# Performance work log

Hardware: AMD Instinct MI355X
Metric: run time of the kernel (lower is better)

## Reference

```python
import jax, jax.numpy as jnp
import numpy as np

D_MODEL = 1024
N_HEADS = 16
D_HEAD = 64
BATCH = 4
SEQ = 2048
NEG = -1000000000.0


def setup_inputs() -> dict:
    key = jax.random.key(0)
    k1, k2, k3, k4, k5 = jax.random.split(key, 5)
    x = jax.random.normal(k1, (BATCH, SEQ, D_MODEL), dtype=jnp.float32)
    std = 0.02
    wq = jax.random.normal(k2, (N_HEADS, D_HEAD, D_MODEL), dtype=jnp.float32) * std
    wk = jax.random.normal(k3, (N_HEADS, D_HEAD, D_MODEL), dtype=jnp.float32) * std
    wv = jax.random.normal(k4, (N_HEADS, D_HEAD, D_MODEL), dtype=jnp.float32) * std
    wo = jax.random.normal(k5, (D_MODEL, N_HEADS * D_HEAD), dtype=jnp.float32) * std
    return {"x": x, "wq": wq, "wk": wk, "wv": wv, "wo": wo}


def reference(x, wq, wk, wv, wo):
    # x: [b, s, d_model]; wq/wk/wv: [h, d_head, d_model]; wo: [d_model, h*d_head]
    b, s, _ = x.shape
    scale = jnp.sqrt(jnp.asarray(D_HEAD, x.dtype))
    q = jnp.einsum('bsd,hed->bhse', x, wq)
    k = jnp.einsum('bsd,hed->bhse', x, wk)
    v = jnp.einsum('bsd,hed->bhse', x, wv)
    scores = jnp.einsum('bhse,bhte->bhst', q, k) / scale
    causal_mask = jnp.triu(jnp.ones((s, s), dtype=bool), k=1)
    scores = jnp.where(causal_mask, jnp.asarray(NEG, scores.dtype), scores)
    weights = jax.nn.softmax(scores, axis=-1)
    heads = jnp.einsum('bhst,bhte->bhse', weights, v)  # [b, h, s, d_head]
    concat = heads.transpose(0, 2, 1, 3).reshape(b, s, N_HEADS * D_HEAD)
    return concat @ wo.T
```

## Files before the change

### kernel.cpp

```cpp
#include <hip/hip_runtime.h>


#define DEV __device__ __forceinline__

typedef __attribute__((ext_vector_type(8))) __bf16 bf16x8;
typedef __attribute__((ext_vector_type(4))) float f32x4;
typedef unsigned short u16;

struct alignas(8) U16x4 { u16 x, y, z, w; };

DEV u16 f2bf(float f) {
  unsigned int u = __builtin_bit_cast(unsigned int, f);
  u = u + 0x7FFFu + ((u >> 16) & 1u);
  return (u16)(u >> 16);
}

DEV unsigned cvt_pk_bf16(float a, float b) {
  unsigned r;
  asm("v_cvt_pk_bf16_f32 %0, %1, %2" : "=v"(r) : "v"(a), "v"(b));
  return r;
}

DEV void gload_lds16(const void* g, void* l) {
  __builtin_amdgcn_global_load_lds(
      (const __attribute__((address_space(1))) unsigned int*)g,
      (__attribute__((address_space(3))) unsigned int*)l, 16, 0, 0);
}

__global__ void cast_kernel(const float* __restrict__ in, u16* __restrict__ out, int n4) {
  int i = blockIdx.x * blockDim.x + threadIdx.x;
  if (i >= n4) return;
  const float4 v = reinterpret_cast<const float4*>(in)[i];
  U16x4 o{f2bf(v.x), f2bf(v.y), f2bf(v.z), f2bf(v.w)};
  reinterpret_cast<U16x4*>(out)[i] = o;
}

__global__ void cast_w_kernel(const float* __restrict__ wq, const float* __restrict__ wk,
                              const float* __restrict__ wv, const float* __restrict__ wo,
                              u16* __restrict__ wqkvb, u16* __restrict__ wob) {
  const int y = blockIdx.y;
  const int i = blockIdx.x * blockDim.x + threadIdx.x;
  const float* src = (y == 0) ? wq : (y == 1) ? wk : (y == 2) ? wv : wo;
  u16* dst = (y < 3) ? (wqkvb + (size_t)y * 1048576) : wob;
  const float4 v = reinterpret_cast<const float4*>(src)[i];
  U16x4 o{f2bf(v.x), f2bf(v.y), f2bf(v.z), f2bf(v.w)};
  reinterpret_cast<U16x4*>(dst)[i] = o;
}

template <int MODE>
__global__ __launch_bounds__(256) void gemm_bt(
    const u16* __restrict__ A, const u16* __restrict__ B,
    void* __restrict__ C0, u16* __restrict__ vtp, int N) {
  constexpr int K = 1024;
  const int bm = blockIdx.y, bn = blockIdx.x;
  const int tid = threadIdx.x;
  const int w = tid >> 6, lane = tid & 63, lo = lane & 15, hi = lane >> 4;
  const int wm = w >> 1, wn = w & 1;

  __shared__ char lds[65536];
  char* sA = lds;
  char* sB = lds + 32768;

  const u16* Ag = A + (size_t)(bm * 128) * K;
  const u16* Bg = B + (size_t)(bn * 128) * K;

  f32x4 acc[4][4] = {};

  auto stage = [&](int buf, int k0) {
#pragma unroll
    for (int it = 0; it < 4; ++it) {
      const int L = (it * 4 + w) * 64 + lane;
      const int r = L >> 3, p = L & 7, c = p ^ (r & 7);
      gload_lds16(Ag + (size_t)r * K + k0 + c * 8, sA + buf * 16384 + (it * 4 + w) * 1024);
      gload_lds16(Bg + (size_t)r * K + k0 + c * 8, sB + buf * 16384 + (it * 4 + w) * 1024);
    }
  };

  stage(0, 0);
  __syncthreads();
  int cur = 0;
  for (int t = 0; t < 16; ++t) {
    if (t + 1 < 16) stage(cur ^ 1, (t + 1) * 64);
#pragma unroll
    for (int kc = 0; kc < 2; ++kc) {
      bf16x8 af[4], bfr[4];
#pragma unroll
      for (int m = 0; m < 4; ++m) {
        const int r = wm * 64 + m * 16 + lo;
        const int p = (kc * 4 + hi) ^ (r & 7);
        af[m] = *reinterpret_cast<const bf16x8*>(sA + cur * 16384 + r * 128 + p * 16);
      }
#pragma unroll
      for (int n = 0; n < 4; ++n) {
        const int r = wn * 64 + n * 16 + lo;
        const int p = (kc * 4 + hi) ^ (r & 7);
        bfr[n] = *reinterpret_cast<const bf16x8*>(sB + cur * 16384 + r * 128 + p * 16);
      }
#pragma unroll
      for (int m = 0; m < 4; ++m)
#pragma unroll
        for (int n = 0; n < 4; ++n)
          acc[m][n] = __builtin_amdgcn_mfma_f32_16x16x32_bf16(af[m], bfr[n], acc[m][n], 0, 0, 0);
    }
    __syncthreads();
    cur ^= 1;
  }

  const int colW = bn * 128 + wn * 64;
  const int rowW = bm * 128 + wm * 64;
  if (MODE == 0) {
    float* C = (float*)C0;
#pragma unroll
    for (int m = 0; m < 4; ++m)
#pragma unroll
      for (int n = 0; n < 4; ++n) {
        const int col = colW + n * 16 + lo;
        const int rb = rowW + m * 16 + hi * 4;
#pragma unroll
        for (int rg = 0; rg < 4; ++rg)
          C[(size_t)(rb + rg) * N + col] = acc[m][n][rg];
      }
  } else {
    u16* qkvp = (u16*)C0;
    if (bn * 128 < 2048) {
      const float qs = (bn < 8) ? 0.18033688011112042f : 1.0f;
#pragma unroll
      for (int m = 0; m < 4; ++m)
#pragma unroll
        for (int n = 0; n < 4; ++n) {
          const int col = colW + n * 16 + lo;
          const int rb = rowW + m * 16 + hi * 4;
#pragma unroll
          for (int rg = 0; rg < 4; ++rg)
            qkvp[(size_t)(rb + rg) * 2048 + col] = f2bf(acc[m][n][rg] * qs);
        }
    } else {
#pragma unroll
      for (int m = 0; m < 4; ++m)
#pragma unroll
        for (int n = 0; n < 4; ++n) {
          const int col = colW + n * 16 + lo;
          const int idx = col - 2048;
          const int hh = idx >> 6, e = idx & 63;
          const int rb = rowW + m * 16 + hi * 4;
          const int bb = rb >> 11, s = rb & 2047;
          U16x4 v4{f2bf(acc[m][n][0]), f2bf(acc[m][n][1]),
                   f2bf(acc[m][n][2]), f2bf(acc[m][n][3])};
          *reinterpret_cast<U16x4*>(vtp + ((size_t)((bb * 16 + hh) * 64 + e)) * 2048 + s) = v4;
        }
    }
  }
}

__global__ __launch_bounds__(256, 4) void attn_kernel(
    const u16* __restrict__ qkv, const u16* __restrict__ vt, u16* __restrict__ heads) {
  const int bx = blockIdx.x;
  const int bh = blockIdx.y;
  const int b = bh >> 4, h = bh & 15;
  const int tid = threadIdx.x;
  const int w = tid >> 6, lane = tid & 63, lo = lane & 15, hi = lane >> 4;

  __shared__ char lds[40960];
  char* sQP = lds;
  char* sK  = lds + 8192;
  char* sV  = lds + 24576;

  const u16* Kg = qkv + (size_t)(b * 2048) * 2048 + 1024 + h * 64;
  const u16* Vg = vt + (size_t)bh * 64 * 2048;

  auto stageKV = [&](int buf, int kv0) {
#pragma unroll
    for (int it = 0; it < 2; ++it) {
      const int L = (it * 4 + w) * 64 + lane;
      const int r = L >> 3, p = L & 7, c = p ^ (r & 7);
      gload_lds16(Kg + (size_t)(kv0 + r) * 2048 + c * 8, sK + buf * 8192 + (it * 4 + w) * 1024);
      gload_lds16(Vg + (size_t)r * 2048 + kv0 + c * 8, sV + buf * 8192 + (it * 4 + w) * 1024);
    }
  };

  char* sP = sQP + w * 2048;

  for (int rep = 0; rep < 2; ++rep) {
    const int qt = rep ? (31 - bx) : bx;
    const u16* Qg = qkv + (size_t)(b * 2048 + qt * 64) * 2048 + h * 64;

#pragma unroll
    for (int it = 0; it < 2; ++it) {
      const int L = (it * 4 + w) * 64 + lane;
      const int r = L >> 3, p = L & 7, c = p ^ (r & 7);
      gload_lds16(Qg + (size_t)r * 2048 + c * 8, sQP + (it * 4 + w) * 1024);
    }
    stageKV(0, 0);
    __syncthreads();

    bf16x8 qf[2];
#pragma unroll
    for (int kc = 0; kc < 2; ++kc) {
      const int r = w * 16 + lo;
      const int p = (kc * 4 + hi) ^ (r & 7);
      qf[kc] = *reinterpret_cast<const bf16x8*>(sQP + r * 128 + p * 16);
    }
    __syncthreads();

    float mreg = -1e30f, lrow = 0.f;
    f32x4 oacc[4] = {};

    const int nt = qt + 1;
    int cur = 0;
    for (int t = 0; t < nt; ++t) {
      if (t + 1 < nt) stageKV(cur ^ 1, (t + 1) * 64);

      f32x4 sa[4] = {};
#pragma unroll
      for (int kc = 0; kc < 2; ++kc) {
#pragma unroll
        for (int n = 0; n < 4; ++n) {
          const int r = n * 16 + lo;
          const int p = (kc * 4 + hi) ^ (r & 7);
          const bf16x8 kf = *reinterpret_cast<const bf16x8*>(sK + cur * 8192 + r * 128 + p * 16);
          sa[n] = __builtin_amdgcn_mfma_f32_16x16x32_bf16(kf, qf[kc], sa[n], 0, 0, 0);
        }
      }

      if (t == nt - 1) {
        const int q = w * 16 + lo;
#pragma unroll
        for (int n = 0; n < 4; ++n)
#pragma unroll
          for (int rg = 0; rg < 4; ++rg)
            if (n * 16 + hi * 4 + rg > q) sa[n][rg] = -1e9f;
      }

      float pm = sa[0][0];
#pragma unroll
      for (int n = 0; n < 4; ++n)
#pragma unroll
        for (int rg = 0; rg < 4; ++rg) pm = fmaxf(pm, sa[n][rg]);
      pm = fmaxf(pm, __shfl_xor(pm, 16));
      pm = fmaxf(pm, __shfl_xor(pm, 32));
      if (!__all(pm <= mreg + 8.0f)) {
        const float mn = fmaxf(mreg, pm);
        const float alpha = exp2f(mreg - mn);
        mreg = mn;
        lrow *= alpha;
#pragma unroll
        for (int ne = 0; ne < 4; ++ne)
#pragma unroll
          for (int rg = 0; rg < 4; ++rg) oacc[ne][rg] *= alpha;
      }
      float rs = 0.f;
#pragma unroll
      for (int n = 0; n < 4; ++n)
#pragma unroll
        for (int rg = 0; rg < 4; ++rg) {
          const float pv = exp2f(sa[n][rg] - mreg);
          sa[n][rg] = pv;
          rs += pv;
        }
      lrow += rs;

#pragma unroll
      for (int n = 0; n < 4; ++n) {
        const unsigned w0 = cvt_pk_bf16(sa[n][0], sa[n][1]);
        const unsigned w1 = cvt_pk_bf16(sa[n][2], sa[n][3]);
        const int Hp = 2 * (n & 1) + (hi >> 1);
        *reinterpret_cast<uint2*>(sP + (n >> 1) * 1024 + Hp * 256 +
                                  ((lo ^ Hp) << 4) + ((hi & 1) << 3)) = uint2{w0, w1};
      }
      asm volatile("s_waitcnt lgkmcnt(0)" ::: "memory");
      bf16x8 pf[2];
#pragma unroll
      for (int kc = 0; kc < 2; ++kc)
        pf[kc] = *reinterpret_cast<const bf16x8*>(sP + kc * 1024 + hi * 256 + ((lo ^ hi) << 4));

#pragma unroll
      for (int kc = 0; kc < 2; ++kc) {
#pragma unroll
        for (int ne = 0; ne < 4; ++ne) {
          const int r = ne * 16 + lo;
          const int p = (kc * 4 + hi) ^ (r & 7);
          const bf16x8 vf = *reinterpret_cast<const bf16x8*>(sV + cur * 8192 + r * 128 + p * 16);
          oacc[ne] = __builtin_amdgcn_mfma_f32_16x16x32_bf16(vf, pf[kc], oacc[ne], 0, 0, 0);
        }
      }
      __syncthreads();
      cur ^= 1;
    }

    float lsum = lrow;
    lsum += __shfl_xor(lsum, 16);
    lsum += __shfl_xor(lsum, 32);
    const float inv = 1.0f / lsum;
    const int q = qt * 64 + w * 16 + lo;
    u16* dst = heads + (size_t)(b * 2048 + q) * 1024 + h * 64;
#pragma unroll
    for (int ne = 0; ne < 4; ++ne) {
      const unsigned r0 = cvt_pk_bf16(oacc[ne][0] * inv, oacc[ne][1] * inv);
      const unsigned r1 = cvt_pk_bf16(oacc[ne][2] * inv, oacc[ne][3] * inv);
      *reinterpret_cast<uint2*>(dst + ne * 16 + hi * 4) = uint2{r0, r1};
    }
  }
}

extern "C" void kernel_launch(void* const* d_in, const int* in_sizes, int n_in,
                              void* d_out, int out_size, void* d_ws, size_t ws_size,
                              hipStream_t stream) {
  const float* x  = (const float*)d_in[0];
  const float* wq = (const float*)d_in[1];
  const float* wk = (const float*)d_in[2];
  const float* wv = (const float*)d_in[3];
  const float* wo = (const float*)d_in[4];

  char* ws = (char*)d_ws;
  u16* xb    = (u16*)(ws);
  u16* wqkvb = (u16*)(ws + 16777216);
  u16* wob   = (u16*)(ws + 23068672);
  u16* qkv   = (u16*)(ws + 25165824);
  u16* vtp   = (u16*)(ws + 58720256);
  u16* heads = (u16*)(ws + 75497472);

  cast_kernel<<<8192, 256, 0, stream>>>(x, xb, 2097152);
  cast_w_kernel<<<dim3(1024, 4), 256, 0, stream>>>(wq, wk, wv, wo, wqkvb, wob);

  gemm_bt<1><<<dim3(24, 64), 256, 0, stream>>>(xb, wqkvb, qkv, vtp, 3072);
  attn_kernel<<<dim3(16, 64), 256, 0, stream>>>(qkv, vtp, heads);
  gemm_bt<0><<<dim3(8, 64), 256, 0, stream>>>(heads, wob, d_out, nullptr, 1024);
}
```

Baseline: 193.6 us.

## Double attention query tile per block to 128 rows for K/V reuse

Each attention workgroup now processes 128 query rows (32 per wave, two 16-row groups) instead of 64, so every staged K/V tile feeds twice as many MFMAs and global K/V traffic per query is halved. The grid shrinks to 8x64 blocks with paired query tiles for causal load balance, LDS grows to 48KB, and the occupancy hint in launch bounds is dropped. s_setprio is added around the MFMA sections to favor matrix issue. The costs are higher register pressure, fewer blocks (512) that may underfill the GPU, and more masked work on the diagonal tiles.

```diff
diff --git a/kernel.cpp b/kernel.cpp
--- a/kernel.cpp
+++ b/kernel.cpp
@@ -152,7 +152,7 @@
   }
 }
 
-__global__ __launch_bounds__(256, 4) void attn_kernel(
+__global__ __launch_bounds__(256) void attn_kernel(
     const u16* __restrict__ qkv, const u16* __restrict__ vt, u16* __restrict__ heads) {
   const int bx = blockIdx.x;
   const int bh = blockIdx.y;
@@ -160,10 +160,10 @@
   const int tid = threadIdx.x;
   const int w = tid >> 6, lane = tid & 63, lo = lane & 15, hi = lane >> 4;
 
-  __shared__ char lds[40960];
+  __shared__ char lds[49152];
   char* sQP = lds;
-  char* sK  = lds + 8192;
-  char* sV  = lds + 24576;
+  char* sK  = lds + 16384;
+  char* sV  = lds + 32768;
 
   const u16* Kg = qkv + (size_t)(b * 2048) * 2048 + 1024 + h * 64;
   const u16* Vg = vt + (size_t)bh * 64 * 2048;
@@ -178,14 +178,14 @@
     }
   };
 
-  char* sP = sQP + w * 2048;
+  char* sP = sQP + w * 4096;
 
   for (int rep = 0; rep < 2; ++rep) {
-    const int qt = rep ? (31 - bx) : bx;
-    const u16* Qg = qkv + (size_t)(b * 2048 + qt * 64) * 2048 + h * 64;
-
-#pragma unroll
-    for (int it = 0; it < 2; ++it) {
+    const int qt = rep ? (15 - bx) : bx;
+    const u16* Qg = qkv + (size_t)(b * 2048 + qt * 128) * 2048 + h * 64;
+
+#pragma unroll
+    for (int it = 0; it < 4; ++it) {
       const int L = (it * 4 + w) * 64 + lane;
       const int r = L >> 3, p = L & 7, c = p ^ (r & 7);
       gload_lds16(Qg + (size_t)r * 2048 + c * 8, sQP + (it * 4 + w) * 1024);
@@ -193,24 +193,27 @@
     stageKV(0, 0);
     __syncthreads();
 
-    bf16x8 qf[2];
-#pragma unroll
-    for (int kc = 0; kc < 2; ++kc) {
-      const int r = w * 16 + lo;
-      const int p = (kc * 4 + hi) ^ (r & 7);
-      qf[kc] = *reinterpret_cast<const bf16x8*>(sQP + r * 128 + p * 16);
-    }
+    bf16x8 qf[2][2];
+#pragma unroll
+    for (int qg = 0; qg < 2; ++qg)
+#pragma unroll
+      for (int kc = 0; kc < 2; ++kc) {
+        const int r = w * 32 + qg * 16 + lo;
+        const int p = (kc * 4 + hi) ^ (r & 7);
+        qf[qg][kc] = *reinterpret_cast<const bf16x8*>(sQP + r * 128 + p * 16);
+      }
     __syncthreads();
 
-    float mreg = -1e30f, lrow = 0.f;
-    f32x4 oacc[4] = {};
-
-    const int nt = qt + 1;
+    float mreg[2] = {-1e30f, -1e30f}, lrow[2] = {0.f, 0.f};
+    f32x4 oacc[2][4] = {};
+
+    const int nt = 2 * (qt + 1);
     int cur = 0;
     for (int t = 0; t < nt; ++t) {
       if (t + 1 < nt) stageKV(cur ^ 1, (t + 1) * 64);
 
-      f32x4 sa[4] = {};
+      f32x4 sa[2][4] = {};
+      __builtin_amdgcn_s_setprio(1);
 #pragma unroll
       for (int kc = 0; kc < 2; ++kc) {
 #pragma unroll
@@ -218,61 +221,73 @@
           const int r = n * 16 + lo;
           const int p = (kc * 4 + hi) ^ (r & 7);
           const bf16x8 kf = *reinterpret_cast<const bf16x8*>(sK + cur * 8192 + r * 128 + p * 16);
-          sa[n] = __builtin_amdgcn_mfma_f32_16x16x32_bf16(kf, qf[kc], sa[n], 0, 0, 0);
-        }
-      }
-
-      if (t == nt - 1) {
-        const int q = w * 16 + lo;
+          sa[0][n] = __builtin_amdgcn_mfma_f32_16x16x32_bf16(kf, qf[0][kc], sa[0][n], 0, 0, 0);
+          sa[1][n] = __builtin_amdgcn_mfma_f32_16x16x32_bf16(kf, qf[1][kc], sa[1][n], 0, 0, 0);
+        }
+      }
+      __builtin_amdgcn_s_setprio(0);
+
+      if (t >= nt - 2) {
+#pragma unroll
+        for (int qg = 0; qg < 2; ++qg) {
+          const int q = qt * 128 + w * 32 + qg * 16 + lo;
+#pragma unroll
+          for (int n = 0; n < 4; ++n)
+#pragma unroll
+            for (int rg = 0; rg < 4; ++rg)
+              if (t * 64 + n * 16 + hi * 4 + rg > q) sa[qg][n][rg] = -1e9f;
+        }
+      }
+
+#pragma unroll
+      for (int qg = 0; qg < 2; ++qg) {
+        float pm = sa[qg][0][0];
 #pragma unroll
         for (int n = 0; n < 4; ++n)
 #pragma unroll
-          for (int rg = 0; rg < 4; ++rg)
-            if (n * 16 + hi * 4 + rg > q) sa[n][rg] = -1e9f;
-      }
-
-      float pm = sa[0][0];
-#pragma unroll
-      for (int n = 0; n < 4; ++n)
-#pragma unroll
-        for (int rg = 0; rg < 4; ++rg) pm = fmaxf(pm, sa[n][rg]);
-      pm = fmaxf(pm, __shfl_xor(pm, 16));
-      pm = fmaxf(pm, __shfl_xor(pm, 32));
-      if (!__all(pm <= mreg + 8.0f)) {
-        const float mn = fmaxf(mreg, pm);
-        const float alpha = exp2f(mreg - mn);
-        mreg = mn;
-        lrow *= alpha;
-#pragma unroll
-        for (int ne = 0; ne < 4; ++ne)
-#pragma unroll
-          for (int rg = 0; rg < 4; ++rg) oacc[ne][rg] *= alpha;
-      }
-      float rs = 0.f;
-#pragma unroll
-      for (int n = 0; n < 4; ++n)
-#pragma unroll
-        for (int rg = 0; rg < 4; ++rg) {
-          const float pv = exp2f(sa[n][rg] - mreg);
-          sa[n][rg] = pv;
-          rs += pv;
-        }
-      lrow += rs;
-
-#pragma unroll
-      for (int n = 0; n < 4; ++n) {
-        const unsigned w0 = cvt_pk_bf16(sa[n][0], sa[n][1]);
-        const unsigned w1 = cvt_pk_bf16(sa[n][2], sa[n][3]);
-        const int Hp = 2 * (n & 1) + (hi >> 1);
-        *reinterpret_cast<uint2*>(sP + (n >> 1) * 1024 + Hp * 256 +
-                                  ((lo ^ Hp) << 4) + ((hi & 1) << 3)) = uint2{w0, w1};
+          for (int rg = 0; rg < 4; ++rg) pm = fmaxf(pm, sa[qg][n][rg]);
+        pm = fmaxf(pm, __shfl_xor(pm, 16));
+        pm = fmaxf(pm, __shfl_xor(pm, 32));
+        if (!__all(pm <= mreg[qg] + 8.0f)) {
+          const float mn = fmaxf(mreg[qg], pm);
+          const float alpha = exp2f(mreg[qg] - mn);
+          mreg[qg] = mn;
+          lrow[qg] *= alpha;
+#pragma unroll
+          for (int ne = 0; ne < 4; ++ne)
+#pragma unroll
+            for (int rg = 0; rg < 4; ++rg) oacc[qg][ne][rg] *= alpha;
+        }
+        float rs = 0.f;
+#pragma unroll
+        for (int n = 0; n < 4; ++n)
+#pragma unroll
+          for (int rg = 0; rg < 4; ++rg) {
+            const float pv = exp2f(sa[qg][n][rg] - mreg[qg]);
+            sa[qg][n][rg] = pv;
+            rs += pv;
+          }
+        lrow[qg] += rs;
+
+#pragma unroll
+        for (int n = 0; n < 4; ++n) {
+          const unsigned w0 = cvt_pk_bf16(sa[qg][n][0], sa[qg][n][1]);
+          const unsigned w1 = cvt_pk_bf16(sa[qg][n][2], sa[qg][n][3]);
+          const int Hp = 2 * (n & 1) + (hi >> 1);
+          *reinterpret_cast<uint2*>(sP + qg * 2048 + (n >> 1) * 1024 + Hp * 256 +
+                                    ((lo ^ Hp) << 4) + ((hi & 1) << 3)) = uint2{w0, w1};
+        }
       }
       asm volatile("s_waitcnt lgkmcnt(0)" ::: "memory");
-      bf16x8 pf[2];
-#pragma unroll
-      for (int kc = 0; kc < 2; ++kc)
-        pf[kc] = *reinterpret_cast<const bf16x8*>(sP + kc * 1024 + hi * 256 + ((lo ^ hi) << 4));
-
+      bf16x8 pf[2][2];
+#pragma unroll
+      for (int qg = 0; qg < 2; ++qg)
+#pragma unroll
+        for (int kc = 0; kc < 2; ++kc)
+          pf[qg][kc] = *reinterpret_cast<const bf16x8*>(
+              sP + qg * 2048 + kc * 1024 + hi * 256 + ((lo ^ hi) << 4));
+
+      __builtin_amdgcn_s_setprio(1);
 #pragma unroll
       for (int kc = 0; kc < 2; ++kc) {
 #pragma unroll
@@ -280,24 +295,29 @@
           const int r = ne * 16 + lo;
           const int p = (kc * 4 + hi) ^ (r & 7);
           const bf16x8 vf = *reinterpret_cast<const bf16x8*>(sV + cur * 8192 + r * 128 + p * 16);
-          oacc[ne] = __builtin_amdgcn_mfma_f32_16x16x32_bf16(vf, pf[kc], oacc[ne], 0, 0, 0);
-        }
-      }
+          oacc[0][ne] = __builtin_amdgcn_mfma_f32_16x16x32_bf16(vf, pf[0][kc], oacc[0][ne], 0, 0, 0);
+          oacc[1][ne] = __builtin_amdgcn_mfma_f32_16x16x32_bf16(vf, pf[1][kc], oacc[1][ne], 0, 0, 0);
+        }
+      }
+      __builtin_amdgcn_s_setprio(0);
       __syncthreads();
       cur ^= 1;
     }
 
-    float lsum = lrow;
-    lsum += __shfl_xor(lsum, 16);
-    lsum += __shfl_xor(lsum, 32);
-    const float inv = 1.0f / lsum;
-    const int q = qt * 64 + w * 16 + lo;
-    u16* dst = heads + (size_t)(b * 2048 + q) * 1024 + h * 64;
-#pragma unroll
-    for (int ne = 0; ne < 4; ++ne) {
-      const unsigned r0 = cvt_pk_bf16(oacc[ne][0] * inv, oacc[ne][1] * inv);
-      const unsigned r1 = cvt_pk_bf16(oacc[ne][2] * inv, oacc[ne][3] * inv);
-      *reinterpret_cast<uint2*>(dst + ne * 16 + hi * 4) = uint2{r0, r1};
+#pragma unroll
+    for (int qg = 0; qg < 2; ++qg) {
+      float lsum = lrow[qg];
+      lsum += __shfl_xor(lsum, 16);
+      lsum += __shfl_xor(lsum, 32);
+      const float inv = 1.0f / lsum;
+      const int q = qt * 128 + w * 32 + qg * 16 + lo;
+      u16* dst = heads + (size_t)(b * 2048 + q) * 1024 + h * 64;
+#pragma unroll
+      for (int ne = 0; ne < 4; ++ne) {
+        const unsigned r0 = cvt_pk_bf16(oacc[qg][ne][0] * inv, oacc[qg][ne][1] * inv);
+        const unsigned r1 = cvt_pk_bf16(oacc[qg][ne][2] * inv, oacc[qg][ne][3] * inv);
+        *reinterpret_cast<uint2*>(dst + ne * 16 + hi * 4) = uint2{r0, r1};
+      }
     }
   }
 }
@@ -323,6 +343,6 @@
   cast_w_kernel<<<dim3(1024, 4), 256, 0, stream>>>(wq, wk, wv, wo, wqkvb, wob);
 
   gemm_bt<1><<<dim3(24, 64), 256, 0, stream>>>(xb, wqkvb, qkv, vtp, 3072);
-  attn_kernel<<<dim3(16, 64), 256, 0, stream>>>(qkv, vtp, heads);
+  attn_kernel<<<dim3(8, 64), 256, 0, stream>>>(qkv, vtp, heads);
   gemm_bt<0><<<dim3(8, 64), 256, 0, stream>>>(heads, wob, d_out, nullptr, 1024);
 }
```

Result: no change. 195.8 us (+1.1%).

## Enlarge attention query tile to 128 rows, remap blocks across XCDs, add setprio

Applied to the files above, without the earlier changes.

The attention kernel moves to 512-thread blocks, each handling a 128-row query tile (8 waves) that shares the K/V tiles staged in LDS, so each K/V load is reused twice as much. Fully masked KV tiles are skipped per wave, and the KV loop is unrolled by two with fixed buffer indices. Both GEMMs and the attention kernel now use a 1D grid with a remapping that groups consecutive logical tiles onto the same XCD, which is meant to improve L2 locality. MFMA sections are wrapped in s_setprio hints. The explicit lgkmcnt wait before reading P back from LDS is removed and left to the compiler, and the larger blocks may reduce occupancy.

```diff
diff --git a/kernel.cpp b/kernel.cpp
--- a/kernel.cpp
+++ b/kernel.cpp
@@ -47,12 +47,15 @@
   reinterpret_cast<U16x4*>(dst)[i] = o;
 }
 
-template <int MODE>
+template <int MODE, int NBN>
 __global__ __launch_bounds__(256) void gemm_bt(
     const u16* __restrict__ A, const u16* __restrict__ B,
     void* __restrict__ C0, u16* __restrict__ vtp, int N) {
   constexpr int K = 1024;
-  const int bm = blockIdx.y, bn = blockIdx.x;
+  const int d = blockIdx.x;
+  const int chunk = gridDim.x >> 3;
+  const int vg = (d & 7) * chunk + (d >> 3);
+  const int bn = vg % NBN, bm = vg / NBN;
   const int tid = threadIdx.x;
   const int w = tid >> 6, lane = tid & 63, lo = lane & 15, hi = lane >> 4;
   const int wm = w >> 1, wn = w & 1;
@@ -152,43 +155,39 @@
   }
 }
 
-__global__ __launch_bounds__(256, 4) void attn_kernel(
+__global__ __launch_bounds__(512, 4) void attn_kernel(
     const u16* __restrict__ qkv, const u16* __restrict__ vt, u16* __restrict__ heads) {
-  const int bx = blockIdx.x;
-  const int bh = blockIdx.y;
+  const int dd = blockIdx.x;
+  const int vg = (dd & 7) * 64 + (dd >> 3);
+  const int bx = vg & 7, bh = vg >> 3;
   const int b = bh >> 4, h = bh & 15;
   const int tid = threadIdx.x;
   const int w = tid >> 6, lane = tid & 63, lo = lane & 15, hi = lane >> 4;
 
-  __shared__ char lds[40960];
+  __shared__ char lds[49152];
   char* sQP = lds;
-  char* sK  = lds + 8192;
-  char* sV  = lds + 24576;
+  char* sK  = lds + 16384;
+  char* sV  = lds + 32768;
 
   const u16* Kg = qkv + (size_t)(b * 2048) * 2048 + 1024 + h * 64;
   const u16* Vg = vt + (size_t)bh * 64 * 2048;
 
+  const int sr = tid >> 3, sc = (tid & 7) ^ (sr & 7);
   auto stageKV = [&](int buf, int kv0) {
+    gload_lds16(Kg + (size_t)(kv0 + sr) * 2048 + sc * 8, sK + buf * 8192 + w * 1024);
+    gload_lds16(Vg + (size_t)sr * 2048 + kv0 + sc * 8, sV + buf * 8192 + w * 1024);
+  };
+
+  char* sP = sQP + w * 2048;
+
+  for (int rep = 0; rep < 2; ++rep) {
+    const int qt = rep ? (15 - bx) : bx;
+    const u16* Qg = qkv + (size_t)(b * 2048 + qt * 128) * 2048 + h * 64;
+
 #pragma unroll
     for (int it = 0; it < 2; ++it) {
-      const int L = (it * 4 + w) * 64 + lane;
-      const int r = L >> 3, p = L & 7, c = p ^ (r & 7);
-      gload_lds16(Kg + (size_t)(kv0 + r) * 2048 + c * 8, sK + buf * 8192 + (it * 4 + w) * 1024);
-      gload_lds16(Vg + (size_t)r * 2048 + kv0 + c * 8, sV + buf * 8192 + (it * 4 + w) * 1024);
-    }
-  };
-
-  char* sP = sQP + w * 2048;
-
-  for (int rep = 0; rep < 2; ++rep) {
-    const int qt = rep ? (31 - bx) : bx;
-    const u16* Qg = qkv + (size_t)(b * 2048 + qt * 64) * 2048 + h * 64;
-
-#pragma unroll
-    for (int it = 0; it < 2; ++it) {
-      const int L = (it * 4 + w) * 64 + lane;
-      const int r = L >> 3, p = L & 7, c = p ^ (r & 7);
-      gload_lds16(Qg + (size_t)r * 2048 + c * 8, sQP + (it * 4 + w) * 1024);
+      const int r = it * 64 + sr;
+      gload_lds16(Qg + (size_t)r * 2048 + sc * 8, sQP + it * 8192 + w * 1024);
     }
     stageKV(0, 0);
     __syncthreads();
@@ -205,93 +204,97 @@
     float mreg = -1e30f, lrow = 0.f;
     f32x4 oacc[4] = {};
 
-    const int nt = qt + 1;
-    int cur = 0;
-    for (int t = 0; t < nt; ++t) {
+    const int nt = 2 * (qt + 1);
+    const int qrow = qt * 128 + w * 16 + lo;
+    const int qmax = qt * 128 + w * 16 + 15;
+
+    auto step = [&](int t, int cur) {
       if (t + 1 < nt) stageKV(cur ^ 1, (t + 1) * 64);
-
-      f32x4 sa[4] = {};
-#pragma unroll
-      for (int kc = 0; kc < 2; ++kc) {
+      if (t * 64 <= qmax) {
+        f32x4 sa[4] = {};
+        __builtin_amdgcn_s_setprio(1);
+#pragma unroll
+        for (int kc = 0; kc < 2; ++kc) {
+#pragma unroll
+          for (int n = 0; n < 4; ++n) {
+            const int r = n * 16 + lo;
+            const int p = (kc * 4 + hi) ^ (lo & 7);
+            const bf16x8 kf = *reinterpret_cast<const bf16x8*>(sK + cur * 8192 + r * 128 + p * 16);
+            sa[n] = __builtin_amdgcn_mfma_f32_16x16x32_bf16(kf, qf[kc], sa[n], 0, 0, 0);
+          }
+        }
+        __builtin_amdgcn_s_setprio(0);
+
+        if (t >= nt - 2) {
+#pragma unroll
+          for (int n = 0; n < 4; ++n)
+#pragma unroll
+            for (int rg = 0; rg < 4; ++rg)
+              if (t * 64 + n * 16 + hi * 4 + rg > qrow) sa[n][rg] = -1e9f;
+        }
+
+        const f32x4 vm2 = __builtin_elementwise_max(__builtin_elementwise_max(sa[0], sa[1]),
+                                                    __builtin_elementwise_max(sa[2], sa[3]));
+        float pm = fmaxf(fmaxf(vm2[0], vm2[1]), fmaxf(vm2[2], vm2[3]));
+        pm = fmaxf(pm, __shfl_xor(pm, 16));
+        pm = fmaxf(pm, __shfl_xor(pm, 32));
+        if (!__all(pm <= mreg + 8.0f)) {
+          const float mn = fmaxf(mreg, pm);
+          const float alpha = exp2f(mreg - mn);
+          mreg = mn;
+          lrow *= alpha;
+#pragma unroll
+          for (int ne = 0; ne < 4; ++ne) oacc[ne] *= alpha;
+        }
+        f32x4 pe[4];
 #pragma unroll
         for (int n = 0; n < 4; ++n) {
-          const int r = n * 16 + lo;
-          const int p = (kc * 4 + hi) ^ (r & 7);
-          const bf16x8 kf = *reinterpret_cast<const bf16x8*>(sK + cur * 8192 + r * 128 + p * 16);
-          sa[n] = __builtin_amdgcn_mfma_f32_16x16x32_bf16(kf, qf[kc], sa[n], 0, 0, 0);
-        }
-      }
-
-      if (t == nt - 1) {
-        const int q = w * 16 + lo;
-#pragma unroll
-        for (int n = 0; n < 4; ++n)
-#pragma unroll
-          for (int rg = 0; rg < 4; ++rg)
-            if (n * 16 + hi * 4 + rg > q) sa[n][rg] = -1e9f;
-      }
-
-      float pm = sa[0][0];
-#pragma unroll
-      for (int n = 0; n < 4; ++n)
-#pragma unroll
-        for (int rg = 0; rg < 4; ++rg) pm = fmaxf(pm, sa[n][rg]);
-      pm = fmaxf(pm, __shfl_xor(pm, 16));
-      pm = fmaxf(pm, __shfl_xor(pm, 32));
-      if (!__all(pm <= mreg + 8.0f)) {
-        const float mn = fmaxf(mreg, pm);
-        const float alpha = exp2f(mreg - mn);
-        mreg = mn;
-        lrow *= alpha;
-#pragma unroll
-        for (int ne = 0; ne < 4; ++ne)
-#pragma unroll
-          for (int rg = 0; rg < 4; ++rg) oacc[ne][rg] *= alpha;
-      }
-      float rs = 0.f;
-#pragma unroll
-      for (int n = 0; n < 4; ++n)
-#pragma unroll
-        for (int rg = 0; rg < 4; ++rg) {
-          const float pv = exp2f(sa[n][rg] - mreg);
-          sa[n][rg] = pv;
-          rs += pv;
-        }
-      lrow += rs;
-
-#pragma unroll
-      for (int n = 0; n < 4; ++n) {
-        const unsigned w0 = cvt_pk_bf16(sa[n][0], sa[n][1]);
-        const unsigned w1 = cvt_pk_bf16(sa[n][2], sa[n][3]);
-        const int Hp = 2 * (n & 1) + (hi >> 1);
-        *reinterpret_cast<uint2*>(sP + (n >> 1) * 1024 + Hp * 256 +
-                                  ((lo ^ Hp) << 4) + ((hi & 1) << 3)) = uint2{w0, w1};
-      }
-      asm volatile("s_waitcnt lgkmcnt(0)" ::: "memory");
-      bf16x8 pf[2];
-#pragma unroll
-      for (int kc = 0; kc < 2; ++kc)
-        pf[kc] = *reinterpret_cast<const bf16x8*>(sP + kc * 1024 + hi * 256 + ((lo ^ hi) << 4));
-
-#pragma unroll
-      for (int kc = 0; kc < 2; ++kc) {
-#pragma unroll
-        for (int ne = 0; ne < 4; ++ne) {
-          const int r = ne * 16 + lo;
-          const int p = (kc * 4 + hi) ^ (r & 7);
-          const bf16x8 vf = *reinterpret_cast<const bf16x8*>(sV + cur * 8192 + r * 128 + p * 16);
-          oacc[ne] = __builtin_amdgcn_mfma_f32_16x16x32_bf16(vf, pf[kc], oacc[ne], 0, 0, 0);
-        }
+          const f32x4 dv = sa[n] - mreg;
+#pragma unroll
+          for (int rg = 0; rg < 4; ++rg) pe[n][rg] = exp2f(dv[rg]);
+        }
+        const f32x4 vs = (pe[0] + pe[1]) + (pe[2] + pe[3]);
+        lrow += (vs[0] + vs[1]) + (vs[2] + vs[3]);
+
+#pragma unroll
+        for (int n = 0; n < 4; ++n) {
+          const unsigned w0 = cvt_pk_bf16(pe[n][0], pe[n][1]);
+          const unsigned w1 = cvt_pk_bf16(pe[n][2], pe[n][3]);
+          const int Hp = 2 * (n & 1) + (hi >> 1);
+          *reinterpret_cast<uint2*>(sP + (n >> 1) * 1024 + Hp * 256 +
+                                    ((lo ^ Hp) << 4) + ((hi & 1) << 3)) = uint2{w0, w1};
+        }
+        bf16x8 pf[2];
+#pragma unroll
+        for (int kc = 0; kc < 2; ++kc)
+          pf[kc] = *reinterpret_cast<const bf16x8*>(sP + kc * 1024 + hi * 256 + ((lo ^ hi) << 4));
+
+        __builtin_amdgcn_s_setprio(1);
+#pragma unroll
+        for (int kc = 0; kc < 2; ++kc) {
+#pragma unroll
+          for (int ne = 0; ne < 4; ++ne) {
+            const int r = ne * 16 + lo;
+            const int p = (kc * 4 + hi) ^ (lo & 7);
+            const bf16x8 vf = *reinterpret_cast<const bf16x8*>(sV + cur * 8192 + r * 128 + p * 16);
+            oacc[ne] = __builtin_amdgcn_mfma_f32_16x16x32_bf16(vf, pf[kc], oacc[ne], 0, 0, 0);
+          }
+        }
+        __builtin_amdgcn_s_setprio(0);
       }
       __syncthreads();
-      cur ^= 1;
+    };
+
+    for (int i = 0; i < nt; i += 2) {
+      step(i, 0);
+      step(i + 1, 1);
     }
 
     float lsum = lrow;
     lsum += __shfl_xor(lsum, 16);
     lsum += __shfl_xor(lsum, 32);
     const float inv = 1.0f / lsum;
-    const int q = qt * 64 + w * 16 + lo;
+    const int q = qt * 128 + w * 16 + lo;
     u16* dst = heads + (size_t)(b * 2048 + q) * 1024 + h * 64;
 #pragma unroll
     for (int ne = 0; ne < 4; ++ne) {
@@ -322,7 +325,7 @@
   cast_kernel<<<8192, 256, 0, stream>>>(x, xb, 2097152);
   cast_w_kernel<<<dim3(1024, 4), 256, 0, stream>>>(wq, wk, wv, wo, wqkvb, wob);
 
-  gemm_bt<1><<<dim3(24, 64), 256, 0, stream>>>(xb, wqkvb, qkv, vtp, 3072);
-  attn_kernel<<<dim3(16, 64), 256, 0, stream>>>(qkv, vtp, heads);
-  gemm_bt<0><<<dim3(8, 64), 256, 0, stream>>>(heads, wob, d_out, nullptr, 1024);
-}
+  gemm_bt<1, 24><<<1536, 256, 0, stream>>>(xb, wqkvb, qkv, vtp, 3072);
+  attn_kernel<<<512, 512, 0, stream>>>(qkv, vtp, heads);
+  gemm_bt<0, 8><<<512, 256, 0, stream>>>(heads, wob, d_out, nullptr, 1024);
+}
```

Measured after the change: 186.5 us. 1.04x faster.
